# Kernel optimization log

Hardware: AMD Instinct MI355X
Metric: run time of the kernel (lower is better)

## Reference

```python
import jax, jax.numpy as jnp
import numpy as np

# BlendParams / camera defaults (pytorch3d)
SIGMA = 1e-4
GAMMA = 1e-4
BG_COLOR = (1.0, 1.0, 1.0)
ZNEAR = 1.0
ZFAR = 100.0
EPS = 1e-10

V, F = 50000, 100000
N, H, W, K = 4, 512, 512, 8


def setup_inputs() -> dict:
    key = jax.random.key(0)
    k1, k2, k3, k4, k5, k6 = jax.random.split(key, 6)
    vn = jax.random.normal(k1, (V, 3), dtype=jnp.float32)
    vn = vn / jnp.linalg.norm(vn, axis=-1, keepdims=True)  # unit vertex normals
    faces = jax.random.randint(k2, (F, 3), 0, V, dtype=jnp.int32)
    # -1 marks empty fragments (background), as in pytorch3d
    pix_to_face = jax.random.randint(k3, (N, H, W, K), -1, F, dtype=jnp.int32)
    bary = jax.random.uniform(k4, (N, H, W, K, 3), dtype=jnp.float32) + 1e-3
    bary = bary / bary.sum(-1, keepdims=True)  # convex barycentric coords
    zbuf = jax.random.uniform(k5, (N, H, W, K), dtype=jnp.float32,
                              minval=ZNEAR, maxval=ZFAR)
    dists = jax.random.normal(k6, (N, H, W, K), dtype=jnp.float32) * 1e-4
    return dict(verts_normals=vn, bary_coords=bary, zbuf=zbuf, dists=dists,
                faces=faces, pix_to_face=pix_to_face)


def reference(verts_normals, bary_coords, zbuf, dists, faces, pix_to_face):
    mask = pix_to_face >= 0                      # [N,H,W,K]
    idx = jnp.where(mask, pix_to_face, 0)
    # phong normal shading: gather per-face vertex normals, bary-interpolate
    face_normals = verts_normals[faces]          # [F,3,3] (3 verts, 3 dims)
    gathered = face_normals[idx]                 # [N,H,W,K,3,3]
    pixel_normals = jnp.einsum('nhwkv,nhwkvc->nhwkc', bary_coords, gathered)
    pixel_normals = jnp.where(mask[..., None], pixel_normals, 0.0)
    # flip y,z and map from [-1,1] to [0,1]
    flip = jnp.array([1.0, -1.0, -1.0], dtype=pixel_normals.dtype)
    colors = (pixel_normals * flip + 1.0) * 0.5  # [N,H,W,K,3]

    # softmax_rgb_blend
    maskf = mask.astype(colors.dtype)
    prob = jax.nn.sigmoid(-dists / SIGMA) * maskf        # [N,H,W,K]
    alpha = 1.0 - jnp.prod(1.0 - prob, axis=-1)          # [N,H,W]
    z_inv = (ZFAR - zbuf) / (ZFAR - ZNEAR) * maskf
    z_inv_max = jnp.maximum(jnp.max(z_inv, axis=-1, keepdims=True), EPS)
    w_num = prob * jnp.exp((z_inv - z_inv_max) / GAMMA)
    delta = jnp.maximum(jnp.exp((EPS - z_inv_max) / GAMMA), EPS)
    denom = jnp.sum(w_num, axis=-1, keepdims=True) + delta  # [N,H,W,1]
    rgb = jnp.einsum('nhwk,nhwkc->nhwc', w_num / denom, colors)
    bg = jnp.array(BG_COLOR, dtype=colors.dtype)
    rgb = rgb + (delta / denom) * bg
    return jnp.concatenate([rgb, (1.0 - alpha)[..., None]], axis=-1)  # [N,H,W,4]
```

## Files before the change

### kernel.cpp

```cpp
#include <hip/hip_runtime.h>


typedef float        f4 __attribute__((ext_vector_type(4)));
typedef int          i4 __attribute__((ext_vector_type(4)));
typedef unsigned int u32;
typedef u32          u4 __attribute__((ext_vector_type(4)));

#define KFRAG 8
#define SIGMA_INV 10000.0f
#define GAMMA_INV 10000.0f
#define ZFAR 100.0f
#define ZRANGE_INV (1.0f / 99.0f)
#define EPSV 1e-10f
#define QSCALE 1023.0f
#define QINV (1.0f / 1023.0f)

__device__ __forceinline__ u32 pack10(float x, float y, float z) {
    u32 qx = (u32)__float2int_rn(__saturatef(x * 0.5f + 0.5f) * QSCALE);
    u32 qy = (u32)__float2int_rn(__saturatef(y * 0.5f + 0.5f) * QSCALE);
    u32 qz = (u32)__float2int_rn(__saturatef(z * 0.5f + 0.5f) * QSCALE);
    return qx | (qy << 10) | (qz << 20);
}

__global__ __launch_bounds__(256) void build_face_tab(
    const float* __restrict__ vn,
    const int*   __restrict__ faces,
    u4*          __restrict__ tab,
    int F)
{
    int f = blockIdx.x * blockDim.x + threadIdx.x;
    if (f >= F) return;
    int v0 = faces[3*f + 0];
    int v1 = faces[3*f + 1];
    int v2 = faces[3*f + 2];
    u4 row;
    row.x = pack10(vn[3*v0], vn[3*v0+1], vn[3*v0+2]);
    row.y = pack10(vn[3*v1], vn[3*v1+1], vn[3*v1+2]);
    row.z = pack10(vn[3*v2], vn[3*v2+1], vn[3*v2+2]);
    row.w = 0;
    tab[f] = row;
}

__global__ __launch_bounds__(256) void soft_phong_kernel(
    const u4*    __restrict__ tab,
    const float* __restrict__ bary,
    const float* __restrict__ zbuf,
    const float* __restrict__ dists,
    const int*   __restrict__ p2f,
    float*       __restrict__ out,
    int P)
{
    int p = blockIdx.x * blockDim.x + threadIdx.x;
    if (p >= P) return;

    const i4* pf4 = (const i4*)(p2f + (size_t)p * KFRAG);
    i4 fa = pf4[0], fb = pf4[1];
    int fk[KFRAG] = {fa.x, fa.y, fa.z, fa.w, fb.x, fb.y, fb.z, fb.w};

    const f4* z4 = (const f4*)(zbuf + (size_t)p * KFRAG);
    f4 za = z4[0], zb = z4[1];
    float zk[KFRAG] = {za.x, za.y, za.z, za.w, zb.x, zb.y, zb.z, zb.w};

    const f4* dd4 = (const f4*)(dists + (size_t)p * KFRAG);
    f4 da = dd4[0], db = dd4[1];
    float dk[KFRAG] = {da.x, da.y, da.z, da.w, db.x, db.y, db.z, db.w};

    const f4* b4 = (const f4*)(bary + (size_t)p * KFRAG * 3);
    float bf[24];
    #pragma unroll
    for (int j = 0; j < 6; j++) {
        f4 t = b4[j];
        bf[4*j+0] = t.x; bf[4*j+1] = t.y; bf[4*j+2] = t.z; bf[4*j+3] = t.w;
    }

    u4 ga[KFRAG];
    #pragma unroll
    for (int k = 0; k < KFRAG; k++) {
        int fi = fk[k] >= 0 ? fk[k] : 0;
        ga[k] = tab[fi];
    }

    float prob[KFRAG], zinv[KFRAG];
    float cr[KFRAG], cg[KFRAG], cb[KFRAG];
    float zmax = EPSV;

    #pragma unroll
    for (int k = 0; k < KFRAG; k++) {
        bool m = (fk[k] >= 0);
        float b0 = bf[3*k + 0], b1 = bf[3*k + 1], b2 = bf[3*k + 2];

        u32 w0 = ga[k].x, w1 = ga[k].y, w2 = ga[k].z;
        float sx = b0 * (float)(w0 & 1023u)
                 + b1 * (float)(w1 & 1023u)
                 + b2 * (float)(w2 & 1023u);
        float sy = b0 * (float)((w0 >> 10) & 1023u)
                 + b1 * (float)((w1 >> 10) & 1023u)
                 + b2 * (float)((w2 >> 10) & 1023u);
        float sz = b0 * (float)(w0 >> 20)
                 + b1 * (float)(w1 >> 20)
                 + b2 * (float)(w2 >> 20);
        cr[k] = sx * QINV;
        cg[k] = 1.0f - sy * QINV;
        cb[k] = 1.0f - sz * QINV;

        prob[k] = m ? (1.0f / (1.0f + __expf(dk[k] * SIGMA_INV))) : 0.0f;
        zinv[k] = m ? ((ZFAR - zk[k]) * ZRANGE_INV) : 0.0f;
        zmax = fmaxf(zmax, zinv[k]);
    }

    float delta = fmaxf(__expf((EPSV - zmax) * GAMMA_INV), EPSV);
    float denom = delta;
    float wr = 0.0f, wg = 0.0f, wb = 0.0f;
    float trans = 1.0f;

    #pragma unroll
    for (int k = 0; k < KFRAG; k++) {
        float w = prob[k] * __expf((zinv[k] - zmax) * GAMMA_INV);
        denom += w;
        wr += w * cr[k];
        wg += w * cg[k];
        wb += w * cb[k];
        trans *= (1.0f - prob[k]);
    }

    float inv = 1.0f / denom;
    f4 o = {(wr + delta) * inv, (wg + delta) * inv, (wb + delta) * inv, trans};
    __builtin_nontemporal_store(o, (f4*)out + p);
}

extern "C" void kernel_launch(void* const* d_in, const int* in_sizes, int n_in,
                              void* d_out, int out_size, void* d_ws, size_t ws_size,
                              hipStream_t stream) {
    const float* vn    = (const float*)d_in[0];
    const float* bary  = (const float*)d_in[1];
    const float* zbuf  = (const float*)d_in[2];
    const float* dists = (const float*)d_in[3];
    const int*   faces = (const int*)d_in[4];
    const int*   p2f   = (const int*)d_in[5];
    float* out = (float*)d_out;

    int P = in_sizes[2] / KFRAG;
    int F = in_sizes[4] / 3;

    u4* tab = (u4*)d_ws;
    int block = 256;
    build_face_tab<<<(F + block - 1) / block, block, 0, stream>>>(
        vn, faces, tab, F);
    soft_phong_kernel<<<(P + block - 1) / block, block, 0, stream>>>(
        tab, bary, zbuf, dists, p2f, out, P);
}
```

Baseline: 243.0 us.

## Map one thread per fragment and reduce across 8 lanes with shuffles

Replaces the per-pixel thread, which looped over 8 fragments, with one thread per fragment. The per-pixel max, weighted sums and transmittance product are combined across groups of 8 lanes with xor shuffles, and lane 0 of each group writes the result. Loads from zbuf, dists, p2f and bary become fully coalesced scalar loads, and there are eight times more threads to hide gather latency. In exchange it adds shuffle instructions, computes the exp in delta only on lane 0, and leaves 7 of 8 lanes idle at the store. The early return is safe only because PK is a multiple of 8.

```diff
diff --git a/kernel.cpp b/kernel.cpp
--- a/kernel.cpp
+++ b/kernel.cpp
@@ -2,7 +2,6 @@
 
 
 typedef float        f4 __attribute__((ext_vector_type(4)));
-typedef int          i4 __attribute__((ext_vector_type(4)));
 typedef unsigned int u32;
 typedef u32          u4 __attribute__((ext_vector_type(4)));
 
@@ -41,91 +40,69 @@
     tab[f] = row;
 }
 
-__global__ __launch_bounds__(256) void soft_phong_kernel(
+__global__ __launch_bounds__(256) void soft_phong_frag(
     const u4*    __restrict__ tab,
     const float* __restrict__ bary,
     const float* __restrict__ zbuf,
     const float* __restrict__ dists,
     const int*   __restrict__ p2f,
     float*       __restrict__ out,
-    int P)
+    int PK)
 {
-    int p = blockIdx.x * blockDim.x + threadIdx.x;
-    if (p >= P) return;
+    int t = blockIdx.x * blockDim.x + threadIdx.x;
+    if (t >= PK) return;
 
-    const i4* pf4 = (const i4*)(p2f + (size_t)p * KFRAG);
-    i4 fa = pf4[0], fb = pf4[1];
-    int fk[KFRAG] = {fa.x, fa.y, fa.z, fa.w, fb.x, fb.y, fb.z, fb.w};
+    int   f   = p2f[t];
+    u4    row = tab[f >= 0 ? f : 0];
+    float z   = zbuf[t];
+    float d   = dists[t];
+    const float* bp = bary + (size_t)t * 3;
+    float b0 = bp[0], b1 = bp[1], b2 = bp[2];
 
-    const f4* z4 = (const f4*)(zbuf + (size_t)p * KFRAG);
-    f4 za = z4[0], zb = z4[1];
-    float zk[KFRAG] = {za.x, za.y, za.z, za.w, zb.x, zb.y, zb.z, zb.w};
+    bool  m    = (f >= 0);
+    float prob = m ? (1.0f / (1.0f + __expf(d * SIGMA_INV))) : 0.0f;
+    float zinv = m ? ((ZFAR - z) * ZRANGE_INV) : 0.0f;
 
-    const f4* dd4 = (const f4*)(dists + (size_t)p * KFRAG);
-    f4 da = dd4[0], db = dd4[1];
-    float dk[KFRAG] = {da.x, da.y, da.z, da.w, db.x, db.y, db.z, db.w};
+    float zmax = fmaxf(zinv, EPSV);
+    zmax = fmaxf(zmax, __shfl_xor(zmax, 1));
+    zmax = fmaxf(zmax, __shfl_xor(zmax, 2));
+    zmax = fmaxf(zmax, __shfl_xor(zmax, 4));
 
-    const f4* b4 = (const f4*)(bary + (size_t)p * KFRAG * 3);
-    float bf[24];
+    u32 w0 = row.x, w1 = row.y, w2 = row.z;
+    float sx = b0 * (float)(w0 & 1023u)
+             + b1 * (float)(w1 & 1023u)
+             + b2 * (float)(w2 & 1023u);
+    float sy = b0 * (float)((w0 >> 10) & 1023u)
+             + b1 * (float)((w1 >> 10) & 1023u)
+             + b2 * (float)((w2 >> 10) & 1023u);
+    float sz = b0 * (float)(w0 >> 20)
+             + b1 * (float)(w1 >> 20)
+             + b2 * (float)(w2 >> 20);
+    float cr = sx * QINV;
+    float cg = 1.0f - sy * QINV;
+    float cb = 1.0f - sz * QINV;
+
+    float w  = prob * __expf((zinv - zmax) * GAMMA_INV);
+    float sw = w, swr = w * cr, swg = w * cg, swb = w * cb;
+    float tr = 1.0f - prob;
     #pragma unroll
-    for (int j = 0; j < 6; j++) {
-        f4 t = b4[j];
-        bf[4*j+0] = t.x; bf[4*j+1] = t.y; bf[4*j+2] = t.z; bf[4*j+3] = t.w;
+    for (int s = 1; s <= 4; s <<= 1) {
+        sw  += __shfl_xor(sw,  s);
+        swr += __shfl_xor(swr, s);
+        swg += __shfl_xor(swg, s);
+        swb += __shfl_xor(swb, s);
+        tr  *= __shfl_xor(tr,  s);
     }
 
-    u4 ga[KFRAG];
-    #pragma unroll
-    for (int k = 0; k < KFRAG; k++) {
-        int fi = fk[k] >= 0 ? fk[k] : 0;
-        ga[k] = tab[fi];
+    if ((threadIdx.x & 7) == 0) {
+        float delta = fmaxf(__expf((EPSV - zmax) * GAMMA_INV), EPSV);
+        float inv   = 1.0f / (sw + delta);
+        f4 o = {(swr + delta) * inv,
+                (swg + delta) * inv,
+                (swb + delta) * inv,
+                tr};
+        __builtin_nontemporal_store(o, (f4*)out + (t >> 3));
     }
-
-    float prob[KFRAG], zinv[KFRAG];
-    float cr[KFRAG], cg[KFRAG], cb[KFRAG];
-    float zmax = EPSV;
-
-    #pragma unroll
-    for (int k = 0; k < KFRAG; k++) {
-        bool m = (fk[k] >= 0);
-        float b0 = bf[3*k + 0], b1 = bf[3*k + 1], b2 = bf[3*k + 2];
-
-        u32 w0 = ga[k].x, w1 = ga[k].y, w2 = ga[k].z;
-        float sx = b0 * (float)(w0 & 1023u)
-                 + b1 * (float)(w1 & 1023u)
-                 + b2 * (float)(w2 & 1023u);
-        float sy = b0 * (float)((w0 >> 10) & 1023u)
-                 + b1 * (float)((w1 >> 10) & 1023u)
-                 + b2 * (float)((w2 >> 10) & 1023u);
-        float sz = b0 * (float)(w0 >> 20)
-                 + b1 * (float)(w1 >> 20)
-                 + b2 * (float)(w2 >> 20);
-        cr[k] = sx * QINV;
-        cg[k] = 1.0f - sy * QINV;
-        cb[k] = 1.0f - sz * QINV;
-
-        prob[k] = m ? (1.0f / (1.0f + __expf(dk[k] * SIGMA_INV))) : 0.0f;
-        zinv[k] = m ? ((ZFAR - zk[k]) * ZRANGE_INV) : 0.0f;
-        zmax = fmaxf(zmax, zinv[k]);
-    }
-
-    float delta = fmaxf(__expf((EPSV - zmax) * GAMMA_INV), EPSV);
-    float denom = delta;
-    float wr = 0.0f, wg = 0.0f, wb = 0.0f;
-    float trans = 1.0f;
-
-    #pragma unroll
-    for (int k = 0; k < KFRAG; k++) {
-        float w = prob[k] * __expf((zinv[k] - zmax) * GAMMA_INV);
-        denom += w;
-        wr += w * cr[k];
-        wg += w * cg[k];
-        wb += w * cb[k];
-        trans *= (1.0f - prob[k]);
-    }
-
-    float inv = 1.0f / denom;
-    f4 o = {(wr + delta) * inv, (wg + delta) * inv, (wb + delta) * inv, trans};
-    __builtin_nontemporal_store(o, (f4*)out + p);
 }
 
 extern "C" void kernel_launch(void* const* d_in, const int* in_sizes, int n_in,
@@ -139,13 +116,13 @@
     const int*   p2f   = (const int*)d_in[5];
     float* out = (float*)d_out;
 
-    int P = in_sizes[2] / KFRAG;
-    int F = in_sizes[4] / 3;
+    int PK = in_sizes[2];
+    int F  = in_sizes[4] / 3;
 
     u4* tab = (u4*)d_ws;
     int block = 256;
     build_face_tab<<<(F + block - 1) / block, block, 0, stream>>>(
         vn, faces, tab, F);
-    soft_phong_kernel<<<(P + block - 1) / block, block, 0, stream>>>(
-        tab, bary, zbuf, dists, p2f, out, P);
+    soft_phong_frag<<<(PK + block - 1) / block, block, 0, stream>>>(
+        tab, bary, zbuf, dists, p2f, out, PK);
 }
```

New measurement: 268.3 us. 10.4% more time.
